# Kernel tuning notes

Hardware: AMD Instinct MI355X
Metric: run time of the kernel (lower is better)

## Reference

```python
import jax, jax.numpy as jnp
import numpy as np

N, E, F, H, C, G = 100000, 1000000, 64, 64, 10, 256


def setup_inputs() -> dict:
    key = jax.random.key(0)
    ks = jax.random.split(key, 16)
    s = 1.0 / np.sqrt(F)
    sh = 1.0 / np.sqrt(H)
    return {
        "x": jax.random.normal(ks[0], (N, F), dtype=jnp.float32),
        "edge_index": jax.random.randint(ks[1], (2, E), 0, N, dtype=jnp.int32),
        "edge_attr": jax.random.uniform(ks[2], (E,), dtype=jnp.float32),
        "batch": jnp.sort(jax.random.randint(ks[3], (N,), 0, G, dtype=jnp.int32)),
        "W1r": jax.random.uniform(ks[4], (F, H), minval=-s, maxval=s),
        "W1s": jax.random.uniform(ks[5], (F, H), minval=-s, maxval=s),
        "b1": jax.random.uniform(ks[6], (H,), minval=-s, maxval=s),
        "W2r": jax.random.uniform(ks[7], (H, H), minval=-sh, maxval=sh),
        "W2s": jax.random.uniform(ks[8], (H, H), minval=-sh, maxval=sh),
        "b2": jax.random.uniform(ks[9], (H,), minval=-sh, maxval=sh),
        "W3r": jax.random.uniform(ks[10], (H, H), minval=-sh, maxval=sh),
        "W3s": jax.random.uniform(ks[11], (H, H), minval=-sh, maxval=sh),
        "b3": jax.random.uniform(ks[12], (H,), minval=-sh, maxval=sh),
        "Wl": jax.random.uniform(ks[13], (H, C), minval=-sh, maxval=sh),
        "bl": jax.random.uniform(ks[14], (C,), minval=-sh, maxval=sh),
    }


def graph_conv(x, src, dst, ew, W_rel, W_root, b):
    # gather neighbor feats, weight per-edge, scatter-add to destination
    msgs = x[src] * ew[:, None]                              # [E, F]
    agg = jax.ops.segment_sum(msgs, dst, num_segments=N)     # [N, F]
    return agg @ W_rel + x @ W_root + b                      # [N, H]


def reference(x, edge_index, edge_attr, batch,
              W1r, W1s, b1, W2r, W2s, b2, W3r, W3s, b3, Wl, bl):
    src, dst = edge_index[0], edge_index[1]
    h = jax.nn.relu(graph_conv(x, src, dst, edge_attr, W1r, W1s, b1))
    h = jax.nn.relu(graph_conv(h, src, dst, edge_attr, W2r, W2s, b2))
    h = jax.nn.relu(graph_conv(h, src, dst, edge_attr, W3r, W3s, b3))
    # global mean pool over graphs in the batch
    sums = jax.ops.segment_sum(h, batch, num_segments=G)      # [G, H]
    cnts = jax.ops.segment_sum(jnp.ones((N,), h.dtype), batch, num_segments=G)
    pooled = sums / jnp.maximum(cnts, 1.0)[:, None]
    # dropout is identity in eval mode
    return pooled @ Wl + bl                                   # [G, C]
```

## Files before the change

kernel.cpp:

```cpp
#include <hip/hip_runtime.h>


#define GCN_F 64
#define GCN_C 10
#define CB_SHIFT 9
#define CB_NODES 512
#define NCB_MAX 200
#define CAP 7168
#define SC_CHUNK 2048

typedef __attribute__((ext_vector_type(8))) short bf16x8;
typedef __attribute__((ext_vector_type(4))) float f32x4;

__device__ __forceinline__ unsigned short f2b(float v) {
    union { float f; unsigned int u; } c; c.f = v;
    unsigned int u = c.u;
    return (unsigned short)((u + 0x7FFFu + ((u >> 16) & 1u)) >> 16);
}
__device__ __forceinline__ float b2f(unsigned short u) {
    union { unsigned int u; float f; } c; c.u = ((unsigned int)u) << 16; return c.f;
}

__global__ __launch_bounds__(256) void zero_kernel(int* __restrict__ p, int n) {
    int i = blockIdx.x * 256 + threadIdx.x;
    if (i < n) p[i] = 0;
}

__global__ __launch_bounds__(256) void histC_kernel(const int* __restrict__ dst,
                                                    int* __restrict__ bcnt,
                                                    int E, int NCB) {
    __shared__ int h[NCB_MAX];
    int tid = threadIdx.x;
    for (int i = tid; i < NCB; i += 256) h[i] = 0;
    __syncthreads();
    int e0 = blockIdx.x * 4096 + tid;
#pragma unroll
    for (int k = 0; k < 16; ++k) {
        int e = e0 + k * 256;
        if (e < E) atomicAdd(&h[dst[e] >> CB_SHIFT], 1);
    }
    __syncthreads();
    for (int i = tid; i < NCB; i += 256)
        if (h[i]) atomicAdd(&bcnt[i], h[i]);
}

__global__ void bscan_kernel(const int* __restrict__ bcnt, int* __restrict__ gstart,
                             int nb) {
    int lane = threadIdx.x;
    int carry = 0;
    for (int base = 0; base < nb; base += 64) {
        int i = base + lane;
        int v = (i < nb) ? bcnt[i] : 0;
        int sc = v;
#pragma unroll
        for (int off = 1; off < 64; off <<= 1) {
            int t = __shfl_up(sc, off);
            if (lane >= off) sc += t;
        }
        if (i < nb) gstart[i] = carry + sc - v;
        carry += __shfl(sc, 63);
    }
    if (lane == 0) gstart[nb] = carry;
}

__global__ __launch_bounds__(256) void scatterC_kernel(
    const int* __restrict__ src, const int* __restrict__ dst,
    const float* __restrict__ ew, const int* __restrict__ gstart,
    int* __restrict__ gcursor, int2* __restrict__ ebufA, int E, int NCB) {
    __shared__ int2 recS[SC_CHUNK];
    __shared__ int gdest[SC_CHUNK];
    __shared__ int hist[NCB_MAX];
    __shared__ int lstart[NCB_MAX];
    __shared__ int gbase[NCB_MAX];
    __shared__ int cur[NCB_MAX];
    __shared__ int sb[256];

    int tid = threadIdx.x;
    int base = blockIdx.x * SC_CHUNK;
    int m = min(SC_CHUNK, E - base);

    for (int i = tid; i < NCB; i += 256) hist[i] = 0;
    __syncthreads();

    int2 rec[8];
    int bk[8];
#pragma unroll
    for (int k = 0; k < 8; ++k) {
        int e = base + k * 256 + tid;
        if (e < E) {
            int d = dst[e];
            bk[k] = d >> CB_SHIFT;
            rec[k] = make_int2(src[e] | ((d & (CB_NODES - 1)) << 17),
                               __float_as_int(ew[e]));
            atomicAdd(&hist[bk[k]], 1);
        } else bk[k] = -1;
    }
    __syncthreads();

    int v = (tid < NCB) ? hist[tid] : 0;
    sb[tid] = v;
    __syncthreads();
    for (int o = 1; o < 256; o <<= 1) {
        int t = (tid >= o) ? sb[tid - o] : 0;
        __syncthreads();
        sb[tid] += t;
        __syncthreads();
    }
    if (tid < NCB) {
        int excl = sb[tid] - v;
        lstart[tid] = excl;
        cur[tid] = excl;
        gbase[tid] = (v > 0) ? atomicAdd(&gcursor[tid], v) : 0;
    }
    __syncthreads();

#pragma unroll
    for (int k = 0; k < 8; ++k) {
        if (bk[k] >= 0) {
            int p = atomicAdd(&cur[bk[k]], 1);
            recS[p] = rec[k];
            gdest[p] = gstart[bk[k]] + gbase[bk[k]] + (p - lstart[bk[k]]);
        }
    }
    __syncthreads();

    for (int i = tid; i < m; i += 256) ebufA[gdest[i]] = recS[i];
}

__global__ __launch_bounds__(256) void sortCB_kernel(
    const int2* __restrict__ ebufA, const int* __restrict__ gstart,
    int2* __restrict__ ebufS, int* __restrict__ offsets, int N, int E) {
    __shared__ int2 rec[CAP];
    __shared__ int cnt[CB_NODES];
    __shared__ int cur[CB_NODES];
    __shared__ int sbuf[256];
    int cb = blockIdx.x, tid = threadIdx.x;
    int e0 = gstart[cb], e1 = gstart[cb + 1];
    int m = min(e1 - e0, CAP);

    for (int i = tid; i < m; i += 256) rec[i] = ebufA[e0 + i];
    for (int i = tid; i < CB_NODES; i += 256) cnt[i] = 0;
    __syncthreads();
    for (int i = tid; i < m; i += 256)
        atomicAdd(&cnt[(unsigned)rec[i].x >> 17], 1);
    __syncthreads();

    int c0 = cnt[2 * tid], c1 = cnt[2 * tid + 1];
    int part = c0 + c1;
    sbuf[tid] = part;
    __syncthreads();
    for (int off = 1; off < 256; off <<= 1) {
        int t = (tid >= off) ? sbuf[tid - off] : 0;
        __syncthreads();
        sbuf[tid] += t;
        __syncthreads();
    }
    int excl = sbuf[tid] - part;
    int pre0 = excl, pre1 = excl + c0;
    cur[2 * tid] = pre0;
    cur[2 * tid + 1] = pre1;
    int g0 = cb * CB_NODES + 2 * tid;
    if (g0 <= N)     offsets[g0]     = e0 + pre0;
    if (g0 + 1 <= N) offsets[g0 + 1] = e0 + pre1;
    __syncthreads();

    for (int i = tid; i < m; i += 256) {
        int d9 = (unsigned)rec[i].x >> 17;
        int pos = atomicAdd(&cur[d9], 1);
        ebufS[e0 + pos] = make_int2(rec[i].x & 0x1FFFF, rec[i].y);
    }
}

__global__ __launch_bounds__(256) void cvt_kernel(const float* __restrict__ in,
                                                  unsigned short* __restrict__ out,
                                                  int n4) {
    int stride = gridDim.x * blockDim.x;
    for (int i = blockIdx.x * blockDim.x + threadIdx.x; i < n4; i += stride) {
        float4 v = reinterpret_cast<const float4*>(in)[i];
        ushort4 o;
        o.x = f2b(v.x); o.y = f2b(v.y); o.z = f2b(v.z); o.w = f2b(v.w);
        reinterpret_cast<ushort4*>(out)[i] = o;
    }
}

__global__ __launch_bounds__(256) void spmm8_kernel(
    const unsigned short* __restrict__ xin, const int* __restrict__ offsets,
    const int2* __restrict__ ebufS, unsigned short* __restrict__ aggOut, int n)
{
    int tid = threadIdx.x, lane = tid & 63, wave = tid >> 6;
    int l8 = lane & 7;
    int gbase = (lane & 56) << 2;
    int nbase0 = (blockIdx.x * 4 + wave) * 8;
    int nstride = gridDim.x * 32;

    for (int nb = nbase0; nb < n; nb += nstride) {
        int node = nb + (lane >> 3);
        bool nv = node < n;
        int p0 = 0, p1 = 0;
        if (nv) { p0 = offsets[node]; p1 = offsets[node + 1]; }
        float acc[8] = {0.f, 0.f, 0.f, 0.f, 0.f, 0.f, 0.f, 0.f};

        int idx = p0 + l8;
        bool v = idx < p1;
        if (__any(v)) {
            int2 er = ebufS[v ? idx : 0];
            int s  = v ? er.x : 0;
            int wb = v ? er.y : 0;

            for (int c = 1;; ++c) {
                int idxn = p0 + c * 8 + l8;
                bool vn = idxn < p1;
                int2 ern = ebufS[vn ? idxn : 0];

                int sj[8], wj[8];
#pragma unroll
                for (int j = 0; j < 8; ++j) {
                    sj[j] = __builtin_amdgcn_ds_bpermute(gbase + (j << 2), s);
                    wj[j] = __builtin_amdgcn_ds_bpermute(gbase + (j << 2), wb);
                }
                int4 r[8];
#pragma unroll
                for (int j = 0; j < 8; ++j)
                    r[j] = *reinterpret_cast<const int4*>(
                        xin + ((size_t)sj[j] << 6) + l8 * 8);
#pragma unroll
                for (int j = 0; j < 8; ++j) {
                    float wf = __int_as_float(wj[j]);
                    acc[0] = fmaf(__int_as_float(r[j].x << 16),        wf, acc[0]);
                    acc[1] = fmaf(__int_as_float(r[j].x & 0xFFFF0000), wf, acc[1]);
                    acc[2] = fmaf(__int_as_float(r[j].y << 16),        wf, acc[2]);
                    acc[3] = fmaf(__int_as_float(r[j].y & 0xFFFF0000), wf, acc[3]);
                    acc[4] = fmaf(__int_as_float(r[j].z << 16),        wf, acc[4]);
                    acc[5] = fmaf(__int_as_float(r[j].z & 0xFFFF0000), wf, acc[5]);
                    acc[6] = fmaf(__int_as_float(r[j].w << 16),        wf, acc[6]);
                    acc[7] = fmaf(__int_as_float(r[j].w & 0xFFFF0000), wf, acc[7]);
                }

                if (!__any(vn)) break;
                s  = vn ? ern.x : 0;
                wb = vn ? ern.y : 0;
            }
        }

        if (nv) {
            int4 o;
            o.x = (int)f2b(acc[0]) | ((int)f2b(acc[1]) << 16);
            o.y = (int)f2b(acc[2]) | ((int)f2b(acc[3]) << 16);
            o.z = (int)f2b(acc[4]) | ((int)f2b(acc[5]) << 16);
            o.w = (int)f2b(acc[6]) | ((int)f2b(acc[7]) << 16);
            *reinterpret_cast<int4*>(aggOut + ((size_t)node << 6) + l8 * 8) = o;
        }
    }
}

__global__ __launch_bounds__(256) void gemm_kernel(
    const unsigned short* __restrict__ agg, const unsigned short* __restrict__ xin,
    const float* __restrict__ Wr, const float* __restrict__ Ws,
    const float* __restrict__ b, unsigned short* __restrict__ out, int n)
{
    __shared__ __align__(16) unsigned short bfrag[2][2][4][64][8];
    int tid = threadIdx.x;
    for (int i = tid; i < 8192; i += 256) {
        int op = i >> 12;
        int ks = (i >> 11) & 1;
        int ct = (i >> 9) & 3;
        int l  = (i >> 3) & 63;
        int j  = i & 7;
        int k   = ks * 32 + (l >> 4) * 8 + j;
        int col = ct * 16 + (l & 15);
        const float* W = op ? Ws : Wr;
        ((unsigned short*)bfrag)[i] = f2b(W[k * GCN_F + col]);
    }
    __syncthreads();

    int lane = tid & 63, wave = tid >> 6;
    int l15 = lane & 15, lhi = lane >> 4;

    bf16x8 B[2][2][4];
#pragma unroll
    for (int op = 0; op < 2; ++op)
#pragma unroll
        for (int ks = 0; ks < 2; ++ks)
#pragma unroll
            for (int ct = 0; ct < 4; ++ct)
                B[op][ks][ct] = *reinterpret_cast<const bf16x8*>(&bfrag[op][ks][ct][lane][0]);

    float bias[4];
#pragma unroll
    for (int ct = 0; ct < 4; ++ct) bias[ct] = b[ct * 16 + l15];

    int ntiles = (n + 15) >> 4;
    for (int t = blockIdx.x * 4 + wave; t < ntiles; t += gridDim.x * 4) {
        int row = t * 16 + l15;
        int arow = min(row, n - 1);
        const unsigned short* ap = agg + (size_t)arow * GCN_F + lhi * 8;
        const unsigned short* xp = xin + (size_t)arow * GCN_F + lhi * 8;
        bf16x8 a0 = *reinterpret_cast<const bf16x8*>(ap);
        bf16x8 a1 = *reinterpret_cast<const bf16x8*>(ap + 32);
        bf16x8 x0 = *reinterpret_cast<const bf16x8*>(xp);
        bf16x8 x1 = *reinterpret_cast<const bf16x8*>(xp + 32);
#pragma unroll
        for (int ct = 0; ct < 4; ++ct) {
            f32x4 acc = {0.f, 0.f, 0.f, 0.f};
            acc = __builtin_amdgcn_mfma_f32_16x16x32_bf16(a0, B[0][0][ct], acc, 0, 0, 0);
            acc = __builtin_amdgcn_mfma_f32_16x16x32_bf16(a1, B[0][1][ct], acc, 0, 0, 0);
            acc = __builtin_amdgcn_mfma_f32_16x16x32_bf16(x0, B[1][0][ct], acc, 0, 0, 0);
            acc = __builtin_amdgcn_mfma_f32_16x16x32_bf16(x1, B[1][1][ct], acc, 0, 0, 0);
            int col = ct * 16 + l15;
#pragma unroll
            for (int r = 0; r < 4; ++r) {
                int orow = t * 16 + lhi * 4 + r;
                if (orow < n) {
                    float v = fmaxf(acc[r] + bias[ct], 0.f);
                    out[(size_t)orow * GCN_F + col] = f2b(v);
                }
            }
        }
    }
}

__global__ __launch_bounds__(256) void pool_kernel(
    const unsigned short* __restrict__ h, const int* __restrict__ batch,
    const float* __restrict__ Wl, const float* __restrict__ bl,
    float* __restrict__ out, int n)
{
    int g    = blockIdx.x;
    int tid  = threadIdx.x;
    int lane = tid & 63;
    int wave = tid >> 6;

    int i0, i1;
    {
        int lo = 0, hi = n;
        while (lo < hi) { int mid = (lo + hi) >> 1; if (batch[mid] < g) lo = mid + 1; else hi = mid; }
        i0 = lo;
        lo = i0; hi = n;
        while (lo < hi) { int mid = (lo + hi) >> 1; if (batch[mid] < g + 1) lo = mid + 1; else hi = mid; }
        i1 = lo;
    }

    float s = 0.f;
    for (int i = i0 + wave; i < i1; i += 4) s += b2f(h[(size_t)i * GCN_F + lane]);

    __shared__ float sp[4][GCN_F];
    sp[wave][lane] = s;
    __syncthreads();
    if (wave == 0) {
        float tot = sp[0][lane] + sp[1][lane] + sp[2][lane] + sp[3][lane];
        float cntf = (float)(i1 - i0);
        sp[0][lane] = tot / fmaxf(cntf, 1.f);
    }
    __syncthreads();
    if (tid < GCN_C) {
        float o = bl[tid];
#pragma unroll
        for (int j = 0; j < GCN_F; ++j) o += sp[0][j] * Wl[j * GCN_C + tid];
        out[g * GCN_C + tid] = o;
    }
}

extern "C" void kernel_launch(void* const* d_in, const int* in_sizes, int n_in,
                              void* d_out, int out_size, void* d_ws, size_t ws_size,
                              hipStream_t stream) {
    const float* x     = (const float*)d_in[0];
    const int*   ei    = (const int*)d_in[1];
    const float* ew    = (const float*)d_in[2];
    const int*   batch = (const int*)d_in[3];
    const float* W1r   = (const float*)d_in[4];
    const float* W1s   = (const float*)d_in[5];
    const float* b1    = (const float*)d_in[6];
    const float* W2r   = (const float*)d_in[7];
    const float* W2s   = (const float*)d_in[8];
    const float* b2    = (const float*)d_in[9];
    const float* W3r   = (const float*)d_in[10];
    const float* W3s   = (const float*)d_in[11];
    const float* b3    = (const float*)d_in[12];
    const float* Wl    = (const float*)d_in[13];
    const float* bl    = (const float*)d_in[14];
    float* out = (float*)d_out;

    const int N = in_sizes[0] / GCN_F;
    const int E = in_sizes[2];
    const int G = out_size / GCN_C;
    const int NCB = (N + CB_NODES - 1) / CB_NODES;

    const int* src = ei;
    const int* dst = ei + E;

    char* ws = (char*)d_ws;
    size_t off = 0;
    size_t csz = ((size_t)NCB * 4 + 15) & ~(size_t)15;
    int* bcnt    = (int*)(ws + off);  off += csz;
    int* gcursor = (int*)(ws + off);  off += csz;
    int* gstart  = (int*)(ws + off);  off += ((size_t)(NCB + 1) * 4 + 15) & ~(size_t)15;
    int* offsets = (int*)(ws + off);  off += ((size_t)(N + 1) * 4 + 15) & ~(size_t)15;
    int2* ebufA  = (int2*)(ws + off); off += (size_t)E * 8;
    int2* ebufS  = (int2*)(ws + off); off += (size_t)E * 8;
    unsigned short* buf0 = (unsigned short*)(ws + off); off += (size_t)N * GCN_F * 2;
    unsigned short* buf1 = (unsigned short*)(ws + off); off += (size_t)N * GCN_F * 2;
    unsigned short* aggB = (unsigned short*)(ws + off); off += (size_t)N * GCN_F * 2;

    int hblocks = (E + 4095) / 4096;
    int sblocks = (E + SC_CHUNK - 1) / SC_CHUNK;
    int zcount  = (int)(csz * 2 / 4);

    zero_kernel<<<(zcount + 255) / 256, 256, 0, stream>>>(bcnt, zcount);
    histC_kernel<<<hblocks, 256, 0, stream>>>(dst, bcnt, E, NCB);
    bscan_kernel<<<1, 64, 0, stream>>>(bcnt, gstart, NCB);
    scatterC_kernel<<<sblocks, 256, 0, stream>>>(src, dst, ew, gstart, gcursor, ebufA, E, NCB);
    sortCB_kernel<<<NCB, 256, 0, stream>>>(ebufA, gstart, ebufS, offsets, N, E);

    cvt_kernel<<<1024, 256, 0, stream>>>(x, buf0, N * GCN_F / 4);

    const int SBLK = 4096, GBLK = 1563;
    spmm8_kernel<<<SBLK, 256, 0, stream>>>(buf0, offsets, ebufS, aggB, N);
    gemm_kernel<<<GBLK, 256, 0, stream>>>(aggB, buf0, W1r, W1s, b1, buf1, N);
    spmm8_kernel<<<SBLK, 256, 0, stream>>>(buf1, offsets, ebufS, aggB, N);
    gemm_kernel<<<GBLK, 256, 0, stream>>>(aggB, buf1, W2r, W2s, b2, buf0, N);
    spmm8_kernel<<<SBLK, 256, 0, stream>>>(buf0, offsets, ebufS, aggB, N);
    gemm_kernel<<<GBLK, 256, 0, stream>>>(aggB, buf0, W3r, W3s, b3, buf1, N);

    pool_kernel<<<G, 256, 0, stream>>>(buf1, batch, Wl, bl, out, N);
}
```

Measured before the change: 262.7 us.

## Fuse SpMM aggregation with MFMA GEMM per layer and merge zeroing into convert

Each GraphConv layer now runs as one kernel. Every wave aggregates 16 nodes into a shared-memory tile and then runs the bf16 MFMA GEMM with bias and ReLU on that tile, so the aggregated features no longer go to global memory and come back. The zero-init kernel is folded into the fp32-to-bf16 convert kernel, which now runs before the preprocessing. Together this removes three launches, plus the write and re-read of an N x 64 intermediate per layer. In exchange every block reloads and converts the weight fragments (1563 blocks), there is no grid-stride loop, and the per-wave work is fixed, so load imbalance from node degree may show up.

```diff
diff --git a/kernel.cpp b/kernel.cpp
--- a/kernel.cpp
+++ b/kernel.cpp
@@ -21,9 +21,18 @@
     union { unsigned int u; float f; } c; c.u = ((unsigned int)u) << 16; return c.f;
 }
 
-__global__ __launch_bounds__(256) void zero_kernel(int* __restrict__ p, int n) {
-    int i = blockIdx.x * 256 + threadIdx.x;
-    if (i < n) p[i] = 0;
+__global__ __launch_bounds__(256) void cvtz_kernel(const float* __restrict__ in,
+                                                   unsigned short* __restrict__ out,
+                                                   int n4, int* __restrict__ zp, int zn) {
+    int gid = blockIdx.x * 256 + threadIdx.x;
+    if (gid < zn) zp[gid] = 0;
+    int stride = gridDim.x * 256;
+    for (int i = gid; i < n4; i += stride) {
+        float4 v = reinterpret_cast<const float4*>(in)[i];
+        ushort4 o;
+        o.x = f2b(v.x); o.y = f2b(v.y); o.z = f2b(v.z); o.w = f2b(v.w);
+        reinterpret_cast<ushort4*>(out)[i] = o;
+    }
 }
 
 __global__ __launch_bounds__(256) void histC_kernel(const int* __restrict__ dst,
@@ -171,30 +180,37 @@
     }
 }
 
-__global__ __launch_bounds__(256) void cvt_kernel(const float* __restrict__ in,
-                                                  unsigned short* __restrict__ out,
-                                                  int n4) {
-    int stride = gridDim.x * blockDim.x;
-    for (int i = blockIdx.x * blockDim.x + threadIdx.x; i < n4; i += stride) {
-        float4 v = reinterpret_cast<const float4*>(in)[i];
-        ushort4 o;
-        o.x = f2b(v.x); o.y = f2b(v.y); o.z = f2b(v.z); o.w = f2b(v.w);
-        reinterpret_cast<ushort4*>(out)[i] = o;
-    }
-}
-
-__global__ __launch_bounds__(256) void spmm8_kernel(
+__global__ __launch_bounds__(256) void layer_kernel(
     const unsigned short* __restrict__ xin, const int* __restrict__ offsets,
-    const int2* __restrict__ ebufS, unsigned short* __restrict__ aggOut, int n)
+    const int2* __restrict__ ebufS, const float* __restrict__ Wr,
+    const float* __restrict__ Ws, const float* __restrict__ b,
+    unsigned short* __restrict__ out, int n)
 {
+    __shared__ __align__(16) unsigned short bfrag[2][2][4][64][8];
+    __shared__ __align__(16) unsigned short aggS[4][16][72];
     int tid = threadIdx.x, lane = tid & 63, wave = tid >> 6;
+
+    for (int i = tid; i < 8192; i += 256) {
+        int op = i >> 12;
+        int ks = (i >> 11) & 1;
+        int ct = (i >> 9) & 3;
+        int l  = (i >> 3) & 63;
+        int j  = i & 7;
+        int k   = ks * 32 + (l >> 4) * 8 + j;
+        int col = ct * 16 + (l & 15);
+        const float* W = op ? Ws : Wr;
+        ((unsigned short*)bfrag)[i] = f2b(W[k * GCN_F + col]);
+    }
+    __syncthreads();
+
     int l8 = lane & 7;
+    int grp = lane >> 3;
     int gbase = (lane & 56) << 2;
-    int nbase0 = (blockIdx.x * 4 + wave) * 8;
-    int nstride = gridDim.x * 32;
-
-    for (int nb = nbase0; nb < n; nb += nstride) {
-        int node = nb + (lane >> 3);
+    int wbase = blockIdx.x * 64 + wave * 16;
+
+#pragma unroll
+    for (int half = 0; half < 2; ++half) {
+        int node = wbase + half * 8 + grp;
         bool nv = node < n;
         int p0 = 0, p1 = 0;
         if (nv) { p0 = offsets[node]; p1 = offsets[node + 1]; }
@@ -242,38 +258,14 @@
             }
         }
 
-        if (nv) {
-            int4 o;
-            o.x = (int)f2b(acc[0]) | ((int)f2b(acc[1]) << 16);
-            o.y = (int)f2b(acc[2]) | ((int)f2b(acc[3]) << 16);
-            o.z = (int)f2b(acc[4]) | ((int)f2b(acc[5]) << 16);
-            o.w = (int)f2b(acc[6]) | ((int)f2b(acc[7]) << 16);
-            *reinterpret_cast<int4*>(aggOut + ((size_t)node << 6) + l8 * 8) = o;
-        }
-    }
-}
-
-__global__ __launch_bounds__(256) void gemm_kernel(
-    const unsigned short* __restrict__ agg, const unsigned short* __restrict__ xin,
-    const float* __restrict__ Wr, const float* __restrict__ Ws,
-    const float* __restrict__ b, unsigned short* __restrict__ out, int n)
-{
-    __shared__ __align__(16) unsigned short bfrag[2][2][4][64][8];
-    int tid = threadIdx.x;
-    for (int i = tid; i < 8192; i += 256) {
-        int op = i >> 12;
-        int ks = (i >> 11) & 1;
-        int ct = (i >> 9) & 3;
-        int l  = (i >> 3) & 63;
-        int j  = i & 7;
-        int k   = ks * 32 + (l >> 4) * 8 + j;
-        int col = ct * 16 + (l & 15);
-        const float* W = op ? Ws : Wr;
-        ((unsigned short*)bfrag)[i] = f2b(W[k * GCN_F + col]);
-    }
-    __syncthreads();
-
-    int lane = tid & 63, wave = tid >> 6;
+        int4 o;
+        o.x = (int)f2b(acc[0]) | ((int)f2b(acc[1]) << 16);
+        o.y = (int)f2b(acc[2]) | ((int)f2b(acc[3]) << 16);
+        o.z = (int)f2b(acc[4]) | ((int)f2b(acc[5]) << 16);
+        o.w = (int)f2b(acc[6]) | ((int)f2b(acc[7]) << 16);
+        *reinterpret_cast<int4*>(&aggS[wave][half * 8 + grp][l8 * 8]) = o;
+    }
+
     int l15 = lane & 15, lhi = lane >> 4;
 
     bf16x8 B[2][2][4];
@@ -289,31 +281,26 @@
 #pragma unroll
     for (int ct = 0; ct < 4; ++ct) bias[ct] = b[ct * 16 + l15];
 
-    int ntiles = (n + 15) >> 4;
-    for (int t = blockIdx.x * 4 + wave; t < ntiles; t += gridDim.x * 4) {
-        int row = t * 16 + l15;
-        int arow = min(row, n - 1);
-        const unsigned short* ap = agg + (size_t)arow * GCN_F + lhi * 8;
-        const unsigned short* xp = xin + (size_t)arow * GCN_F + lhi * 8;
-        bf16x8 a0 = *reinterpret_cast<const bf16x8*>(ap);
-        bf16x8 a1 = *reinterpret_cast<const bf16x8*>(ap + 32);
-        bf16x8 x0 = *reinterpret_cast<const bf16x8*>(xp);
-        bf16x8 x1 = *reinterpret_cast<const bf16x8*>(xp + 32);
-#pragma unroll
-        for (int ct = 0; ct < 4; ++ct) {
-            f32x4 acc = {0.f, 0.f, 0.f, 0.f};
-            acc = __builtin_amdgcn_mfma_f32_16x16x32_bf16(a0, B[0][0][ct], acc, 0, 0, 0);
-            acc = __builtin_amdgcn_mfma_f32_16x16x32_bf16(a1, B[0][1][ct], acc, 0, 0, 0);
-            acc = __builtin_amdgcn_mfma_f32_16x16x32_bf16(x0, B[1][0][ct], acc, 0, 0, 0);
-            acc = __builtin_amdgcn_mfma_f32_16x16x32_bf16(x1, B[1][1][ct], acc, 0, 0, 0);
-            int col = ct * 16 + l15;
-#pragma unroll
-            for (int r = 0; r < 4; ++r) {
-                int orow = t * 16 + lhi * 4 + r;
-                if (orow < n) {
-                    float v = fmaxf(acc[r] + bias[ct], 0.f);
-                    out[(size_t)orow * GCN_F + col] = f2b(v);
-                }
+    bf16x8 a0 = *reinterpret_cast<const bf16x8*>(&aggS[wave][l15][lhi * 8]);
+    bf16x8 a1 = *reinterpret_cast<const bf16x8*>(&aggS[wave][l15][32 + lhi * 8]);
+    const unsigned short* xp = xin + (size_t)min(wbase + l15, n - 1) * GCN_F + lhi * 8;
+    bf16x8 x0 = *reinterpret_cast<const bf16x8*>(xp);
+    bf16x8 x1 = *reinterpret_cast<const bf16x8*>(xp + 32);
+
+#pragma unroll
+    for (int ct = 0; ct < 4; ++ct) {
+        f32x4 acc = {0.f, 0.f, 0.f, 0.f};
+        acc = __builtin_amdgcn_mfma_f32_16x16x32_bf16(a0, B[0][0][ct], acc, 0, 0, 0);
+        acc = __builtin_amdgcn_mfma_f32_16x16x32_bf16(a1, B[0][1][ct], acc, 0, 0, 0);
+        acc = __builtin_amdgcn_mfma_f32_16x16x32_bf16(x0, B[1][0][ct], acc, 0, 0, 0);
+        acc = __builtin_amdgcn_mfma_f32_16x16x32_bf16(x1, B[1][1][ct], acc, 0, 0, 0);
+        int col = ct * 16 + l15;
+#pragma unroll
+        for (int r = 0; r < 4; ++r) {
+            int orow = wbase + lhi * 4 + r;
+            if (orow < n) {
+                float v = fmaxf(acc[r] + bias[ct], 0.f);
+                out[(size_t)orow * GCN_F + col] = f2b(v);
             }
         }
     }
@@ -398,27 +385,21 @@
     int2* ebufS  = (int2*)(ws + off); off += (size_t)E * 8;
     unsigned short* buf0 = (unsigned short*)(ws + off); off += (size_t)N * GCN_F * 2;
     unsigned short* buf1 = (unsigned short*)(ws + off); off += (size_t)N * GCN_F * 2;
-    unsigned short* aggB = (unsigned short*)(ws + off); off += (size_t)N * GCN_F * 2;
 
     int hblocks = (E + 4095) / 4096;
     int sblocks = (E + SC_CHUNK - 1) / SC_CHUNK;
     int zcount  = (int)(csz * 2 / 4);
 
-    zero_kernel<<<(zcount + 255) / 256, 256, 0, stream>>>(bcnt, zcount);
+    cvtz_kernel<<<1024, 256, 0, stream>>>(x, buf0, N * GCN_F / 4, bcnt, zcount);
     histC_kernel<<<hblocks, 256, 0, stream>>>(dst, bcnt, E, NCB);
     bscan_kernel<<<1, 64, 0, stream>>>(bcnt, gstart, NCB);
     scatterC_kernel<<<sblocks, 256, 0, stream>>>(src, dst, ew, gstart, gcursor, ebufA, E, NCB);
     sortCB_kernel<<<NCB, 256, 0, stream>>>(ebufA, gstart, ebufS, offsets, N, E);
 
-    cvt_kernel<<<1024, 256, 0, stream>>>(x, buf0, N * GCN_F / 4);
-
-    const int SBLK = 4096, GBLK = 1563;
-    spmm8_kernel<<<SBLK, 256, 0, stream>>>(buf0, offsets, ebufS, aggB, N);
-    gemm_kernel<<<GBLK, 256, 0, stream>>>(aggB, buf0, W1r, W1s, b1, buf1, N);
-    spmm8_kernel<<<SBLK, 256, 0, stream>>>(buf1, offsets, ebufS, aggB, N);
-    gemm_kernel<<<GBLK, 256, 0, stream>>>(aggB, buf1, W2r, W2s, b2, buf0, N);
-    spmm8_kernel<<<SBLK, 256, 0, stream>>>(buf0, offsets, ebufS, aggB, N);
-    gemm_kernel<<<GBLK, 256, 0, stream>>>(aggB, buf0, W3r, W3s, b3, buf1, N);
+    const int LBLK = (N + 63) / 64;
+    layer_kernel<<<LBLK, 256, 0, stream>>>(buf0, offsets, ebufS, W1r, W1s, b1, buf1, N);
+    layer_kernel<<<LBLK, 256, 0, stream>>>(buf1, offsets, ebufS, W2r, W2s, b2, buf0, N);
+    layer_kernel<<<LBLK, 256, 0, stream>>>(buf0, offsets, ebufS, W3r, W3s, b3, buf1, N);
 
     pool_kernel<<<G, 256, 0, stream>>>(buf1, batch, Wl, bl, out, N);
 }
```

New measurement: 245.3 us. 1.07x faster.
